# Kernel tuning notes

Measured on AMD Instinct MI355X. Metric: run time of the kernel, lower is better.

## Reference

```python
import jax, jax.numpy as jnp
import numpy as np

B, CL, H, W, NP = 128, 8, 16, 16, 32   # batch, primary cap length, height, width, n primary capsules
NC, CLO, ITER = 10, 16, 3              # n output capsules, output capsule length, routing iterations


def squash(t):
    # TensorMONK Activations 'squash': squash along axis 2 of a 3D tensor
    ss = jnp.sum(t * t, axis=2, keepdims=True)
    return (ss / (1.0 + ss)) * t / jnp.sqrt(ss)


def setup_inputs() -> dict:
    key = jax.random.key(0)
    k1, k2 = jax.random.split(key)
    tensor = jax.random.normal(k1, (B, CL, H, W, NP), dtype=jnp.float32)
    # nn.Parameter(torch.randn(...).normal_(0.0, 0.1)) -> N(0, 0.1)
    weight = 0.1 * jax.random.normal(k2, (CL * H * W, NP, NC * CLO), dtype=jnp.float32)
    return {"tensor": tensor, "weight": weight}


def reference(tensor, weight):
    b, cl, h, w, n_prim = tensor.shape
    # flatten spatial/length dims, squash along primary-capsule axis (dim 2, faithful to source)
    x = squash(tensor.reshape(b, -1, n_prim))                  # (B, P, N) with P = cl*h*w
    # (B,P,1,N) @ (P,N,K) broadcasted matmul -> (B,P,K)
    u = jnp.einsum('bpn,pnk->bpk', x, weight)
    u = u.reshape(b, cl, h, w, NC, CLO)                        # (B, cl, h, w, NC, CLO)
    bias = jnp.zeros((b, cl, h, w, NC), dtype=tensor.dtype)
    v = None
    for i in range(ITER):  # fixed small iteration count
        c = jax.nn.softmax(bias, axis=4)                       # softmax over output capsules
        s = jnp.einsum('bchwn,bchwnk->bnk', c, u)              # weighted sum over cl,h,w
        v = squash(s)                                          # squash along capsule length (axis 2)
        if i < ITER - 1:
            bias = bias + jnp.einsum('bchwnk,bnk->bchwn', u, v)
    return v
```

## Files before the change

### kernel.cpp

```cpp
#include <hip/hip_runtime.h>

typedef unsigned short u16;
typedef __attribute__((ext_vector_type(8))) short bf16x8;
typedef __attribute__((ext_vector_type(4))) float f32x4;

#define B_   128
#define P_   2048
#define NC_  10
#define F_   160
#define NBLK 512
#define PPB  4
#define NTHR 512
#define XS   40
#define WS   40

__device__ __forceinline__ u16 f2bf(float f) {
    union { float f; unsigned u; } v; v.f = f;
    unsigned r = v.u + 0x7FFFu + ((v.u >> 16) & 1u);
    return (u16)(r >> 16);
}
__device__ __forceinline__ float bf2f(u16 h) {
    union { unsigned u; float f; } v; v.u = ((unsigned)h) << 16;
    return v.f;
}

__global__ void k_squash_x(const float* __restrict__ t, u16* __restrict__ xb) {
    int g = blockIdx.x * 256 + threadIdx.x;
    int pair = g >> 2, sub = g & 3;
    int p = pair & 2047, b = pair >> 11;
    const float4* tg = (const float4*)t;
    int fi = pair * 8 + sub * 2;
    float4 va = tg[fi], vb = tg[fi + 1];
    float ss = va.x*va.x + va.y*va.y + va.z*va.z + va.w*va.w
             + vb.x*vb.x + vb.y*vb.y + vb.z*vb.z + vb.w*vb.w;
    ss += __shfl_xor(ss, 1);
    ss += __shfl_xor(ss, 2);
    float fct = ss / ((1.f + ss) * sqrtf(ss));
    u16 h[8] __attribute__((aligned(16)));
    h[0]=f2bf(va.x*fct); h[1]=f2bf(va.y*fct); h[2]=f2bf(va.z*fct); h[3]=f2bf(va.w*fct);
    h[4]=f2bf(vb.x*fct); h[5]=f2bf(vb.y*fct); h[6]=f2bf(vb.z*fct); h[7]=f2bf(vb.w*fct);
    *(uint4*)(xb + (p * 128 + b) * 32 + sub * 8) = *(const uint4*)h;
}

__global__ void k_wt(const float* __restrict__ w, u16* __restrict__ wb) {
    __shared__ u16 wl[32 * F_];
    int p = blockIdx.x, tid = threadIdx.x;
    const float4* wp = (const float4*)(w + p * 32 * F_);
    for (int e4 = tid; e4 < 1280; e4 += 256) {
        float4 v = wp[e4];
        u16 h[4] __attribute__((aligned(8)));
        h[0]=f2bf(v.x); h[1]=f2bf(v.y); h[2]=f2bf(v.z); h[3]=f2bf(v.w);
        *(ushort4*)(wl + e4 * 4) = *(const ushort4*)h;
    }
    __syncthreads();
    u16* wo = wb + p * F_ * 32;
    for (int sid = tid; sid < 640; sid += 256) {
        int f = sid >> 2, k0 = (sid & 3) << 3;
        u16 tmp[8] __attribute__((aligned(16)));
#pragma unroll
        for (int j = 0; j < 8; ++j) tmp[j] = wl[(k0 + j) * F_ + f];
        *(uint4*)(wo + f * 32 + k0) = *(const uint4*)tmp;
    }
}

template<int MODE>
__global__ __launch_bounds__(NTHR, 2) void k_pass(
        const u16* __restrict__ xb, const u16* __restrict__ wb,
        const float* __restrict__ vprev, u16* __restrict__ s_part)
{
    __shared__ u16 xt[128 * XS];
    __shared__ u16 wt[F_ * WS];
    const int tid = threadIdx.x, blk = blockIdx.x;
    const int L = tid & 63, wv = tid >> 6;
    const int q = L >> 4, col = L & 15;
    const int b = wv * 16 + col;
    const int p0 = blk * PPB;

    float4 vv[NC_];
    if (MODE != 0) {
#pragma unroll
        for (int n = 0; n < NC_; ++n)
            vv[n] = *(const float4*)(vprev + b * F_ + n * 16 + q * 4);
    }

    f32x4 s_acc[NC_];
#pragma unroll
    for (int n = 0; n < NC_; ++n) s_acc[n] = (f32x4){0.f, 0.f, 0.f, 0.f};

    uint4 r0, r1, r2;
    {
        const uint4* xg = (const uint4*)(xb + p0 * 4096);
        const uint4* wg = (const uint4*)(wb + p0 * 5120);
        r0 = xg[tid]; r1 = wg[tid];
        if (tid < 128) r2 = wg[tid + 512];
    }

#pragma unroll
    for (int pp = 0; pp < PPB; ++pp) {
        __syncthreads();
        *(uint4*)&xt[(tid >> 2) * XS + (tid & 3) * 8] = r0;
        *(uint4*)&wt[(tid >> 2) * WS + (tid & 3) * 8] = r1;
        if (tid < 128)
            *(uint4*)&wt[(128 + (tid >> 2)) * WS + (tid & 3) * 8] = r2;
        if (pp + 1 < PPB) {
            const uint4* xg = (const uint4*)(xb + (p0 + pp + 1) * 4096);
            const uint4* wg = (const uint4*)(wb + (p0 + pp + 1) * 5120);
            r0 = xg[tid]; r1 = wg[tid];
            if (tid < 128) r2 = wg[tid + 512];
        }
        __syncthreads();

        bf16x8 bfrag = *(const bf16x8*)&xt[b * XS + q * 8];
        if (MODE == 0) {
#pragma unroll
            for (int n = 0; n < NC_; ++n) {
                bf16x8 afrag = *(const bf16x8*)&wt[(n * 16 + col) * WS + q * 8];
                s_acc[n] = __builtin_amdgcn_mfma_f32_16x16x32_bf16(afrag, bfrag, s_acc[n], 0, 0, 0);
            }
        } else {
            float tt[NC_];
#pragma unroll
            for (int n = 0; n < NC_; ++n) {
                bf16x8 afrag = *(const bf16x8*)&wt[(n * 16 + col) * WS + q * 8];
                f32x4 z = {0.f, 0.f, 0.f, 0.f};
                f32x4 acc = __builtin_amdgcn_mfma_f32_16x16x32_bf16(afrag, bfrag, z, 0, 0, 0);
                float t = acc[0]*vv[n].x + acc[1]*vv[n].y + acc[2]*vv[n].z + acc[3]*vv[n].w;
                t += __shfl_xor(t, 16);
                t += __shfl_xor(t, 32);
                tt[n] = t;
            }
            float mx = tt[0];
#pragma unroll
            for (int n = 1; n < NC_; ++n) mx = fmaxf(mx, tt[n]);
            float den = 0.f;
#pragma unroll
            for (int n = 0; n < NC_; ++n) { tt[n] = __expf(tt[n] - mx); den += tt[n]; }
            float inv = 1.f / den;
#pragma unroll
            for (int n = 0; n < NC_; ++n) {
                bf16x8 afrag = *(const bf16x8*)&wt[(n * 16 + col) * WS + q * 8];
                f32x4 z = {0.f, 0.f, 0.f, 0.f};
                f32x4 acc = __builtin_amdgcn_mfma_f32_16x16x32_bf16(afrag, bfrag, z, 0, 0, 0);
                float cf = tt[n] * inv;
#pragma unroll
                for (int r = 0; r < 4; ++r) s_acc[n][r] += cf * acc[r];
            }
        }
    }

    u16* sp = s_part + blk * (B_ * F_);
    const float sc = (MODE == 0) ? 0.1f : 1.f;
#pragma unroll
    for (int n = 0; n < NC_; ++n) {
        u16 h[4] __attribute__((aligned(8)));
#pragma unroll
        for (int r = 0; r < 4; ++r) h[r] = f2bf(s_acc[n][r] * sc);
        *(ushort4*)(sp + b * F_ + n * 16 + q * 4) = *(const ushort4*)h;
    }
}

template<int ADD>
__global__ void k_red(const u16* __restrict__ s_part,
                      const float* __restrict__ vprev, float* __restrict__ vout) {
    __shared__ float r0s[256], r1s[256];
    const int tid = threadIdx.x, blk = blockIdx.x;
    const int pid = tid & 31, part = tid >> 5;
    const uint* sp = (const uint*)s_part;
    const int opair = blk * 32 + pid;
    float a0 = 0.f, a1 = 0.f;
#pragma unroll 8
    for (int g = part; g < NBLK; g += 8) {
        uint u = sp[g * 10240 + opair];
        a0 += bf2f((u16)(u & 0xffff));
        a1 += bf2f((u16)(u >> 16));
    }
    r0s[tid] = a0; r1s[tid] = a1;
    __syncthreads();
    if (tid < 32) {
        float s0 = 0.f, s1 = 0.f;
#pragma unroll
        for (int k = 0; k < 8; ++k) { s0 += r0s[k * 32 + tid]; s1 += r1s[k * 32 + tid]; }
        float sq = s0 * s0 + s1 * s1;
        sq += __shfl_xor(sq, 1);
        sq += __shfl_xor(sq, 2);
        sq += __shfl_xor(sq, 4);
        float fct = sq / ((1.f + sq) * sqrtf(sq));
        float2 o = make_float2(s0 * fct, s1 * fct);
        if (ADD) {
            float2 pv = *(const float2*)(vprev + 2 * (blk * 32 + tid));
            o.x += pv.x; o.y += pv.y;
        }
        *(float2*)(vout + 2 * (blk * 32 + tid)) = o;
    }
}

extern "C" void kernel_launch(void* const* d_in, const int* in_sizes, int n_in,
                              void* d_out, int out_size, void* d_ws, size_t ws_size,
                              hipStream_t stream) {
    const float* tensor = (const float*)d_in[0];
    const float* weight = (const float*)d_in[1];
    float* out = (float*)d_out;
    char* ws = (char*)d_ws;

    u16*   xb     = (u16*)(ws);
    u16*   wb     = (u16*)(ws + 16777216);
    u16*   s_part = (u16*)(ws + 37748736);
    float* v0     = (float*)(ws + 58720256);
    float* vs     = (float*)(ws + 58802176);

    k_squash_x<<<4096, 256, 0, stream>>>(tensor, xb);
    k_wt<<<2048, 256, 0, stream>>>(weight, wb);

    k_pass<0><<<NBLK, NTHR, 0, stream>>>(xb, wb, nullptr, s_part);
    k_red<0><<<320, 256, 0, stream>>>(s_part, nullptr, v0);
    k_pass<1><<<NBLK, NTHR, 0, stream>>>(xb, wb, v0, s_part);
    k_red<1><<<320, 256, 0, stream>>>(s_part, v0, vs);
    k_pass<2><<<NBLK, NTHR, 0, stream>>>(xb, wb, vs, s_part);
    k_red<0><<<320, 256, 0, stream>>>(s_part, nullptr, out);
}
```

Measured before the change: 174.1 us.

## Use direct global-to-LDS double buffering with XOR swizzle, merge prep kernels, vectorize reduction

```diff
diff --git a/kernel.cpp b/kernel.cpp
--- a/kernel.cpp
+++ b/kernel.cpp
@@ -1,6 +1,7 @@
 #include <hip/hip_runtime.h>
 
 typedef unsigned short u16;
+typedef unsigned int u32;
 typedef __attribute__((ext_vector_type(8))) short bf16x8;
 typedef __attribute__((ext_vector_type(4))) float f32x4;
 
@@ -11,8 +12,10 @@
 #define NBLK 512
 #define PPB  4
 #define NTHR 512
-#define XS   40
-#define WS   40
+
+#define GLL(g, l) __builtin_amdgcn_global_load_lds( \
+    (const __attribute__((address_space(1))) void*)(g), \
+    (__attribute__((address_space(3))) void*)(l), 16, 0, 0)
 
 __device__ __forceinline__ u16 f2bf(float f) {
     union { float f; unsigned u; } v; v.f = f;
@@ -24,56 +27,61 @@
     return v.f;
 }
 
-__global__ void k_squash_x(const float* __restrict__ t, u16* __restrict__ xb) {
-    int g = blockIdx.x * 256 + threadIdx.x;
-    int pair = g >> 2, sub = g & 3;
-    int p = pair & 2047, b = pair >> 11;
-    const float4* tg = (const float4*)t;
-    int fi = pair * 8 + sub * 2;
-    float4 va = tg[fi], vb = tg[fi + 1];
-    float ss = va.x*va.x + va.y*va.y + va.z*va.z + va.w*va.w
-             + vb.x*vb.x + vb.y*vb.y + vb.z*vb.z + vb.w*vb.w;
-    ss += __shfl_xor(ss, 1);
-    ss += __shfl_xor(ss, 2);
-    float fct = ss / ((1.f + ss) * sqrtf(ss));
-    u16 h[8] __attribute__((aligned(16)));
-    h[0]=f2bf(va.x*fct); h[1]=f2bf(va.y*fct); h[2]=f2bf(va.z*fct); h[3]=f2bf(va.w*fct);
-    h[4]=f2bf(vb.x*fct); h[5]=f2bf(vb.y*fct); h[6]=f2bf(vb.z*fct); h[7]=f2bf(vb.w*fct);
-    *(uint4*)(xb + (p * 128 + b) * 32 + sub * 8) = *(const uint4*)h;
-}
-
-__global__ void k_wt(const float* __restrict__ w, u16* __restrict__ wb) {
+__global__ void k_prep(const float* __restrict__ t, const float* __restrict__ w,
+                       u16* __restrict__ xb, u16* __restrict__ wb) {
     __shared__ u16 wl[32 * F_];
-    int p = blockIdx.x, tid = threadIdx.x;
-    const float4* wp = (const float4*)(w + p * 32 * F_);
-    for (int e4 = tid; e4 < 1280; e4 += 256) {
-        float4 v = wp[e4];
-        u16 h[4] __attribute__((aligned(8)));
-        h[0]=f2bf(v.x); h[1]=f2bf(v.y); h[2]=f2bf(v.z); h[3]=f2bf(v.w);
-        *(ushort4*)(wl + e4 * 4) = *(const ushort4*)h;
-    }
-    __syncthreads();
-    u16* wo = wb + p * F_ * 32;
-    for (int sid = tid; sid < 640; sid += 256) {
-        int f = sid >> 2, k0 = (sid & 3) << 3;
-        u16 tmp[8] __attribute__((aligned(16)));
-#pragma unroll
-        for (int j = 0; j < 8; ++j) tmp[j] = wl[(k0 + j) * F_ + f];
-        *(uint4*)(wo + f * 32 + k0) = *(const uint4*)tmp;
+    const int tid = threadIdx.x;
+    if (blockIdx.x < 4096) {
+        int g = blockIdx.x * 256 + tid;
+        int pair = g >> 2, sub = g & 3;
+        int p = pair & 2047, b = pair >> 11;
+        const float4* tg = (const float4*)t;
+        int fi = pair * 8 + sub * 2;
+        float4 va = tg[fi], vb = tg[fi + 1];
+        float ss = va.x*va.x + va.y*va.y + va.z*va.z + va.w*va.w
+                 + vb.x*vb.x + vb.y*vb.y + vb.z*vb.z + vb.w*vb.w;
+        ss += __shfl_xor(ss, 1);
+        ss += __shfl_xor(ss, 2);
+        float fct = ss / ((1.f + ss) * sqrtf(ss));
+        u16 h[8] __attribute__((aligned(16)));
+        h[0]=f2bf(va.x*fct); h[1]=f2bf(va.y*fct); h[2]=f2bf(va.z*fct); h[3]=f2bf(va.w*fct);
+        h[4]=f2bf(vb.x*fct); h[5]=f2bf(vb.y*fct); h[6]=f2bf(vb.z*fct); h[7]=f2bf(vb.w*fct);
+        int sw = sub ^ ((b >> 1) & 3);
+        *(uint4*)(xb + (p * 128 + b) * 32 + sw * 8) = *(const uint4*)h;
+    } else {
+        int p = blockIdx.x - 4096;
+        const float4* wp = (const float4*)(w + p * 32 * F_);
+        for (int e4 = tid; e4 < 1280; e4 += 256) {
+            float4 v = wp[e4];
+            u16 h[4] __attribute__((aligned(8)));
+            h[0]=f2bf(v.x); h[1]=f2bf(v.y); h[2]=f2bf(v.z); h[3]=f2bf(v.w);
+            *(ushort4*)(wl + e4 * 4) = *(const ushort4*)h;
+        }
+        __syncthreads();
+        u16* wo = wb + p * F_ * 32;
+        for (int sid = tid; sid < 640; sid += 256) {
+            int f = sid >> 2, k0 = (sid & 3) << 3;
+            u16 tmp[8] __attribute__((aligned(16)));
+#pragma unroll
+            for (int j = 0; j < 8; ++j) tmp[j] = wl[(k0 + j) * F_ + f];
+            int sw = (sid & 3) ^ ((f >> 1) & 3);
+            *(uint4*)(wo + f * 32 + sw * 8) = *(const uint4*)tmp;
+        }
     }
 }
 
 template<int MODE>
-__global__ __launch_bounds__(NTHR, 2) void k_pass(
+__global__ __launch_bounds__(NTHR, 4) void k_pass(
         const u16* __restrict__ xb, const u16* __restrict__ wb,
         const float* __restrict__ vprev, u16* __restrict__ s_part)
 {
-    __shared__ u16 xt[128 * XS];
-    __shared__ u16 wt[F_ * WS];
+    __shared__ u16 xt[2][4096];
+    __shared__ u16 wt[2][5120];
     const int tid = threadIdx.x, blk = blockIdx.x;
     const int L = tid & 63, wv = tid >> 6;
     const int q = L >> 4, col = L & 15;
     const int b = wv * 16 + col;
+    const int qs = (q ^ ((col >> 1) & 3)) * 8;
     const int p0 = blk * PPB;
 
     float4 vv[NC_];
@@ -87,41 +95,38 @@
 #pragma unroll
     for (int n = 0; n < NC_; ++n) s_acc[n] = (f32x4){0.f, 0.f, 0.f, 0.f};
 
-    uint4 r0, r1, r2;
     {
-        const uint4* xg = (const uint4*)(xb + p0 * 4096);
-        const uint4* wg = (const uint4*)(wb + p0 * 5120);
-        r0 = xg[tid]; r1 = wg[tid];
-        if (tid < 128) r2 = wg[tid + 512];
-    }
-
+        const u16* xg = xb + (size_t)p0 * 4096;
+        const u16* wg = wb + (size_t)p0 * 5120;
+        GLL(xg + tid * 8, &xt[0][tid * 8]);
+        GLL(wg + tid * 8, &wt[0][tid * 8]);
+        if (tid < 128) GLL(wg + 4096 + tid * 8, &wt[0][4096 + tid * 8]);
+    }
+    __syncthreads();
+
+    int cur = 0;
 #pragma unroll
     for (int pp = 0; pp < PPB; ++pp) {
-        __syncthreads();
-        *(uint4*)&xt[(tid >> 2) * XS + (tid & 3) * 8] = r0;
-        *(uint4*)&wt[(tid >> 2) * WS + (tid & 3) * 8] = r1;
-        if (tid < 128)
-            *(uint4*)&wt[(128 + (tid >> 2)) * WS + (tid & 3) * 8] = r2;
         if (pp + 1 < PPB) {
-            const uint4* xg = (const uint4*)(xb + (p0 + pp + 1) * 4096);
-            const uint4* wg = (const uint4*)(wb + (p0 + pp + 1) * 5120);
-            r0 = xg[tid]; r1 = wg[tid];
-            if (tid < 128) r2 = wg[tid + 512];
-        }
-        __syncthreads();
-
-        bf16x8 bfrag = *(const bf16x8*)&xt[b * XS + q * 8];
+            const u16* xg = xb + (size_t)(p0 + pp + 1) * 4096;
+            const u16* wg = wb + (size_t)(p0 + pp + 1) * 5120;
+            GLL(xg + tid * 8, &xt[cur ^ 1][tid * 8]);
+            GLL(wg + tid * 8, &wt[cur ^ 1][tid * 8]);
+            if (tid < 128) GLL(wg + 4096 + tid * 8, &wt[cur ^ 1][4096 + tid * 8]);
+        }
+
+        bf16x8 bfrag = *(const bf16x8*)&xt[cur][b * 32 + qs];
         if (MODE == 0) {
 #pragma unroll
             for (int n = 0; n < NC_; ++n) {
-                bf16x8 afrag = *(const bf16x8*)&wt[(n * 16 + col) * WS + q * 8];
+                bf16x8 afrag = *(const bf16x8*)&wt[cur][(n * 16 + col) * 32 + qs];
                 s_acc[n] = __builtin_amdgcn_mfma_f32_16x16x32_bf16(afrag, bfrag, s_acc[n], 0, 0, 0);
             }
         } else {
             float tt[NC_];
 #pragma unroll
             for (int n = 0; n < NC_; ++n) {
-                bf16x8 afrag = *(const bf16x8*)&wt[(n * 16 + col) * WS + q * 8];
+                bf16x8 afrag = *(const bf16x8*)&wt[cur][(n * 16 + col) * 32 + qs];
                 f32x4 z = {0.f, 0.f, 0.f, 0.f};
                 f32x4 acc = __builtin_amdgcn_mfma_f32_16x16x32_bf16(afrag, bfrag, z, 0, 0, 0);
                 float t = acc[0]*vv[n].x + acc[1]*vv[n].y + acc[2]*vv[n].z + acc[3]*vv[n].w;
@@ -138,7 +143,7 @@
             float inv = 1.f / den;
 #pragma unroll
             for (int n = 0; n < NC_; ++n) {
-                bf16x8 afrag = *(const bf16x8*)&wt[(n * 16 + col) * WS + q * 8];
+                bf16x8 afrag = *(const bf16x8*)&wt[cur][(n * 16 + col) * 32 + qs];
                 f32x4 z = {0.f, 0.f, 0.f, 0.f};
                 f32x4 acc = __builtin_amdgcn_mfma_f32_16x16x32_bf16(afrag, bfrag, z, 0, 0, 0);
                 float cf = tt[n] * inv;
@@ -146,6 +151,8 @@
                 for (int r = 0; r < 4; ++r) s_acc[n][r] += cf * acc[r];
             }
         }
+        __syncthreads();
+        cur ^= 1;
     }
 
     u16* sp = s_part + blk * (B_ * F_);
@@ -162,24 +169,32 @@
 template<int ADD>
 __global__ void k_red(const u16* __restrict__ s_part,
                       const float* __restrict__ vprev, float* __restrict__ vout) {
-    __shared__ float r0s[256], r1s[256];
+    __shared__ float red[32 * 66];
     const int tid = threadIdx.x, blk = blockIdx.x;
-    const int pid = tid & 31, part = tid >> 5;
-    const uint* sp = (const uint*)s_part;
-    const int opair = blk * 32 + pid;
-    float a0 = 0.f, a1 = 0.f;
-#pragma unroll 8
-    for (int g = part; g < NBLK; g += 8) {
-        uint u = sp[g * 10240 + opair];
-        a0 += bf2f((u16)(u & 0xffff));
-        a1 += bf2f((u16)(u >> 16));
-    }
-    r0s[tid] = a0; r1s[tid] = a1;
+    const int pid = tid & 7, part = tid >> 3;
+    const uint4* sp4 = (const uint4*)s_part;
+    const int base = blk * 8 + pid;
+    float a[8];
+#pragma unroll
+    for (int j = 0; j < 8; ++j) a[j] = 0.f;
+#pragma unroll
+    for (int g = part; g < NBLK; g += 32) {
+        uint4 uv = sp4[g * 2560 + base];
+        a[0] += bf2f((u16)(uv.x & 0xffff)); a[1] += bf2f((u16)(uv.x >> 16));
+        a[2] += bf2f((u16)(uv.y & 0xffff)); a[3] += bf2f((u16)(uv.y >> 16));
+        a[4] += bf2f((u16)(uv.z & 0xffff)); a[5] += bf2f((u16)(uv.z >> 16));
+        a[6] += bf2f((u16)(uv.w & 0xffff)); a[7] += bf2f((u16)(uv.w >> 16));
+    }
+#pragma unroll
+    for (int j = 0; j < 8; ++j) red[part * 66 + pid * 8 + j] = a[j];
     __syncthreads();
     if (tid < 32) {
         float s0 = 0.f, s1 = 0.f;
 #pragma unroll
-        for (int k = 0; k < 8; ++k) { s0 += r0s[k * 32 + tid]; s1 += r1s[k * 32 + tid]; }
+        for (int k = 0; k < 32; ++k) {
+            s0 += red[k * 66 + tid * 2];
+            s1 += red[k * 66 + tid * 2 + 1];
+        }
         float sq = s0 * s0 + s1 * s1;
         sq += __shfl_xor(sq, 1);
         sq += __shfl_xor(sq, 2);
@@ -208,8 +223,7 @@
     float* v0     = (float*)(ws + 58720256);
     float* vs     = (float*)(ws + 58802176);
 
-    k_squash_x<<<4096, 256, 0, stream>>>(tensor, xb);
-    k_wt<<<2048, 256, 0, stream>>>(weight, wb);
+    k_prep<<<6144, 256, 0, stream>>>(tensor, weight, xb, wb);
 
     k_pass<0><<<NBLK, NTHR, 0, stream>>>(xb, wb, nullptr, s_part);
     k_red<0><<<320, 256, 0, stream>>>(s_part, nullptr, v0);
```

Result: slower. 242.8 us (+39.5%).
